# Performance work log

Hardware: AMD Instinct MI355X
Metric: run time of the kernel (lower is better)

Reference implementation:

```python
import jax, jax.numpy as jnp
import numpy as np

DIM = 1024
NUM_HEADS = 16
B, T = 2, 2048


def setup_inputs() -> dict:
    key = jax.random.key(0)
    ks = jax.random.split(key, 7)
    s = 0.02
    return {
        "Q": jax.random.normal(ks[0], (B, T, DIM), dtype=jnp.float32),
        "K": jax.random.normal(ks[1], (B, T, DIM), dtype=jnp.float32),
        "V": jax.random.normal(ks[2], (B, T, DIM), dtype=jnp.float32),
        "Wq": jax.random.normal(ks[3], (DIM, DIM), dtype=jnp.float32) * s,
        "Wk": jax.random.normal(ks[4], (DIM, DIM), dtype=jnp.float32) * s,
        "Wv": jax.random.normal(ks[5], (DIM, DIM), dtype=jnp.float32) * s,
        "Wp": jax.random.normal(ks[6], (DIM, DIM), dtype=jnp.float32) * s,
    }


def _split_heads(x, h):
    b, t, d = x.shape
    return x.reshape(b, t, h, d // h).transpose(0, 2, 1, 3)  # b h t d


def reference(Q, K, V, Wq, Wk, Wv, Wp):
    b, t, d = Q.shape
    h = NUM_HEADS
    # NOTE: module scales by 1/sqrt(dim) (full model dim), not 1/sqrt(head_dim)
    scale = 1.0 / np.sqrt(d).astype(np.float32)
    # torch Linear: x @ W.T (bias=False)
    q = _split_heads(Q @ Wq.T, h)  # b h t hd
    k = _split_heads(K @ Wk.T, h)
    v = _split_heads(V @ Wv.T, h)
    att = jnp.einsum('bhid,bhjd->bhij', q, k) * scale  # b h t t
    causal = jnp.tril(jnp.ones((t, t), dtype=bool))
    att = jnp.where(causal[None, None], att, -jnp.inf)
    att = jax.nn.softmax(att, axis=-1)
    y = jnp.einsum('bhij,bhjd->bhid', att, v)  # b h t hd
    y = y.transpose(0, 2, 1, 3).reshape(b, t, d)
    y = y @ Wp.T
    return (y, att, k, v)
```

## Files before the change

### kernel.cpp

```cpp
#include <hip/hip_runtime.h>

typedef __attribute__((ext_vector_type(8))) short s16x8;
typedef __attribute__((ext_vector_type(4))) float f32x4;

static __device__ __forceinline__ unsigned short f2bf(float f) {
  union { float f; unsigned int u; } v; v.f = f;
  unsigned int u = v.u;
  u += 0x7fffu + ((u >> 16) & 1u);
  return (unsigned short)(u >> 16);
}
static __device__ __forceinline__ void gload16(const void* g, void* l) {
  __builtin_amdgcn_global_load_lds((const __attribute__((address_space(1))) unsigned int*)g,
                                   (__attribute__((address_space(3))) unsigned int*)l, 16, 0, 0);
}

__global__ __launch_bounds__(256) void cast7_bf16(
    const float* __restrict__ i0, const float* __restrict__ i1, const float* __restrict__ i2,
    const float* __restrict__ i3, const float* __restrict__ i4, const float* __restrict__ i5,
    const float* __restrict__ i6,
    unsigned short* __restrict__ o0, unsigned short* __restrict__ o1,
    unsigned short* __restrict__ o2, unsigned short* __restrict__ o3,
    unsigned short* __restrict__ o4, unsigned short* __restrict__ o5,
    unsigned short* __restrict__ o6) {
  const int z = blockIdx.z;
  const float* in = z == 0 ? i0 : z == 1 ? i1 : z == 2 ? i2 : z == 3 ? i3 : z == 4 ? i4
                    : z == 5 ? i5 : i6;
  unsigned short* out = z == 0 ? o0 : z == 1 ? o1 : z == 2 ? o2 : z == 3 ? o3 : z == 4 ? o4
                        : z == 5 ? o5 : o6;
  const int n = (z < 3) ? 4194304 : 1048576;
  int i = (blockIdx.x * 256 + threadIdx.x) * 8;
  if (i >= n) return;
  float4 a = *reinterpret_cast<const float4*>(in + i);
  float4 b = *reinterpret_cast<const float4*>(in + i + 4);
  s16x8 o;
  o[0] = (short)f2bf(a.x); o[1] = (short)f2bf(a.y);
  o[2] = (short)f2bf(a.z); o[3] = (short)f2bf(a.w);
  o[4] = (short)f2bf(b.x); o[5] = (short)f2bf(b.y);
  o[6] = (short)f2bf(b.z); o[7] = (short)f2bf(b.w);
  *reinterpret_cast<s16x8*>(out + i) = o;
}

__global__ __launch_bounds__(256) void gemm_bf16(
    const unsigned short* __restrict__ A0, const unsigned short* __restrict__ A1,
    const unsigned short* __restrict__ A2,
    const unsigned short* __restrict__ W0, const unsigned short* __restrict__ W1,
    const unsigned short* __restrict__ W2,
    unsigned short* __restrict__ Oq, unsigned short* __restrict__ Ok,
    float* __restrict__ Kf, unsigned short* __restrict__ OvT,
    float* __restrict__ Vf, float* __restrict__ Orm) {
  __shared__ __align__(16) char LDS[32768];

  const int z = blockIdx.z;
  const unsigned short* A = z == 0 ? A0 : z == 1 ? A1 : A2;
  const unsigned short* W = z == 0 ? W0 : z == 1 ? W1 : W2;

  const int tid = threadIdx.x, lane = tid & 63, w = tid >> 6;
  const int wm = w >> 1, wn = w & 1;
  const int row0 = blockIdx.y * 128, col0 = blockIdx.x * 128;

  f32x4 acc[4][4];
#pragma unroll
  for (int m = 0; m < 4; ++m)
#pragma unroll
    for (int n = 0; n < 4; ++n) acc[m][n] = f32x4{0.f, 0.f, 0.f, 0.f};

  const int srow = tid >> 3;
  const int swb = ((tid & 7) * 16) ^ ((srow & 7) << 4);
  const unsigned short* aSrc = A + (size_t)(row0 + srow) * 1024 + (swb >> 1);
  const unsigned short* bSrc = W + (size_t)(col0 + srow) * 1024 + (swb >> 1);
  char* ldsA = LDS + w * 1024;
  char* ldsB = LDS + 16384 + w * 1024;

  const int lr = lane & 15, g16 = (lane >> 4) * 16;

  for (int k0 = 0; k0 < 1024; k0 += 64) {
    __syncthreads();
#pragma unroll
    for (int p = 0; p < 4; ++p) gload16(aSrc + (size_t)p * 32 * 1024 + k0, ldsA + p * 4096);
#pragma unroll
    for (int p = 0; p < 4; ++p) gload16(bSrc + (size_t)p * 32 * 1024 + k0, ldsB + p * 4096);
    __syncthreads();

    s16x8 af[2][4], bf[2][4];
#pragma unroll
    for (int ks = 0; ks < 2; ++ks) {
#pragma unroll
      for (int m = 0; m < 4; ++m) {
        int r = wm * 64 + m * 16 + lr;
        int cb = (ks * 64 + g16) ^ ((r & 7) << 4);
        af[ks][m] = *reinterpret_cast<const s16x8*>(LDS + r * 128 + cb);
      }
#pragma unroll
      for (int n = 0; n < 4; ++n) {
        int r = wn * 64 + n * 16 + lr;
        int cb = (ks * 64 + g16) ^ ((r & 7) << 4);
        bf[ks][n] = *reinterpret_cast<const s16x8*>(LDS + 16384 + r * 128 + cb);
      }
    }
#pragma unroll
    for (int ks = 0; ks < 2; ++ks)
#pragma unroll
      for (int m = 0; m < 4; ++m)
#pragma unroll
        for (int n = 0; n < 4; ++n)
          acc[m][n] = __builtin_amdgcn_mfma_f32_16x16x32_bf16(af[ks][m], bf[ks][n], acc[m][n], 0, 0, 0);
  }

  const int er = (lane >> 4) * 4, ec = lane & 15;
  const int b = row0 >> 11, trow = row0 & 2047;

  if (Orm) {
#pragma unroll
    for (int m = 0; m < 4; ++m)
#pragma unroll
      for (int n = 0; n < 4; ++n)
#pragma unroll
        for (int j = 0; j < 4; ++j)
          Orm[(size_t)(row0 + wm * 64 + m * 16 + er + j) * 1024 + col0 + wn * 64 + n * 16 + ec] =
              acc[m][n][j];
    return;
  }

  {
    float* F = (z == 1) ? Kf : (z == 2) ? Vf : nullptr;
    if (F) {
#pragma unroll
      for (int m = 0; m < 4; ++m)
#pragma unroll
        for (int n = 0; n < 4; ++n)
#pragma unroll
          for (int j = 0; j < 4; ++j) {
            int t = trow + wm * 64 + m * 16 + er + j;
            int gd = col0 + wn * 64 + n * 16 + ec;
            F[((size_t)(b * 16 + (gd >> 6)) * 2048 + t) * 64 + (gd & 63)] = acc[m][n][j];
          }
    }
  }

  __syncthreads();
  if (z == 2) {
#pragma unroll
    for (int m = 0; m < 4; ++m)
#pragma unroll
      for (int n = 0; n < 4; ++n)
#pragma unroll
        for (int j = 0; j < 4; ++j) {
          int d = wn * 64 + n * 16 + ec, t = wm * 64 + m * 16 + er + j;
          *reinterpret_cast<short*>(LDS + d * 256 + t * 2) = (short)f2bf(acc[m][n][j]);
        }
    __syncthreads();
    const int dr = tid >> 1, half = tid & 1;
    const int gd = col0 + dr, h = gd >> 6, dd = gd & 63;
    unsigned short* dst = OvT + ((size_t)(b * 16 + h) * 64 + dd) * 2048 + trow + half * 64;
    const char* src = LDS + dr * 256 + half * 128;
#pragma unroll
    for (int i = 0; i < 8; ++i)
      *reinterpret_cast<s16x8*>(dst + i * 8) = *reinterpret_cast<const s16x8*>(src + i * 16);
  } else {
    unsigned short* On = (z == 0) ? Oq : Ok;
#pragma unroll
    for (int m = 0; m < 4; ++m)
#pragma unroll
      for (int n = 0; n < 4; ++n)
#pragma unroll
        for (int j = 0; j < 4; ++j) {
          int r = wm * 64 + m * 16 + er + j, c = wn * 64 + n * 16 + ec;
          *reinterpret_cast<short*>(LDS + r * 256 + c * 2) = (short)f2bf(acc[m][n][j]);
        }
    __syncthreads();
    const int r = tid >> 1, half = tid & 1;
    const int h = (col0 >> 6) + half;
    unsigned short* dst = On + ((size_t)(b * 16 + h) * 2048 + trow + r) * 64;
    const char* src = LDS + r * 256 + half * 128;
#pragma unroll
    for (int i = 0; i < 8; ++i)
      *reinterpret_cast<s16x8*>(dst + i * 8) = *reinterpret_cast<const s16x8*>(src + i * 16);
  }
}

#define ALD 68

__global__ __launch_bounds__(256) void attn_kernel(
    const unsigned short* __restrict__ qw, const unsigned short* __restrict__ kw,
    const unsigned short* __restrict__ vt, float* __restrict__ att_out,
    unsigned short* __restrict__ yb) {
  __shared__ __align__(16) char LDSA[2][16384];
  __shared__ short Pl[4][16 * ALD];

  const int tid = threadIdx.x, lane = tid & 63, w = tid >> 6;
  const int flat = blockIdx.y * 32 + blockIdx.x;
  const int xcd = flat & 7, idx = flat >> 3;
  const int bh = xcd * 4 + (idx >> 5);
  const int iblk = 31 - (idx & 31);
  const float scale2 = 0.03125f * 1.44269504f;

  const int lr = lane & 15, g16 = (lane >> 4) * 16;
  const int lk = (lane >> 4) * 8, er = (lane >> 4) * 4;
  const int rbase = iblk * 64 + w * 16 + er;

  s16x8 aq[2];
  {
    const unsigned short* qb = qw + ((size_t)bh * 2048 + iblk * 64 + w * 16 + lr) * 64;
    aq[0] = *reinterpret_cast<const s16x8*>(qb + lk);
    aq[1] = *reinterpret_cast<const s16x8*>(qb + 32 + lk);
  }

  const int sw = ((lane & 7) * 16) ^ ((lane >> 3) << 4);
  const unsigned short* kLane = kw + (size_t)bh * 131072 + (size_t)(lane >> 3) * 64 + (sw >> 1);
  const unsigned short* vLane = vt + (size_t)bh * 131072 + (size_t)(lane >> 3) * 2048 + (sw >> 1);

  float lrow[4] = {0.f, 0.f, 0.f, 0.f};

  {
    const int npairs = (iblk + 2) >> 1;
#pragma unroll
    for (int i = 0; i < 4; ++i)
      gload16(kLane + (size_t)(w * 32 + i * 8) * 64, LDSA[0] + w * 4096 + i * 1024);
    __syncthreads();
    int buf = 0;
    for (int p = 0; p < npairs; ++p) {
      if (p + 1 < npairs) {
#pragma unroll
        for (int i = 0; i < 4; ++i)
          gload16(kLane + (size_t)((p + 1) * 128 + w * 32 + i * 8) * 64,
                  LDSA[buf ^ 1] + w * 4096 + i * 1024);
      }
#pragma unroll
      for (int sub = 0; sub < 2; ++sub) {
        int jt = 2 * p + sub;
        if (jt > iblk) break;
        const char* Kb = LDSA[buf] + sub * 8192;
        f32x4 s[4];
#pragma unroll
        for (int n = 0; n < 4; ++n) {
          s[n] = f32x4{0.f, 0.f, 0.f, 0.f};
          int r = n * 16 + lr;
#pragma unroll
          for (int ks = 0; ks < 2; ++ks) {
            int cb = (ks * 64 + g16) ^ ((r & 7) << 4);
            s16x8 bK = *reinterpret_cast<const s16x8*>(Kb + r * 128 + cb);
            s[n] = __builtin_amdgcn_mfma_f32_16x16x32_bf16(aq[ks], bK, s[n], 0, 0, 0);
          }
        }
#pragma unroll
        for (int n = 0; n < 4; ++n) {
          int c = jt * 64 + n * 16 + lr;
#pragma unroll
          for (int j = 0; j < 4; ++j) {
            float sv = (c > rbase + j) ? -1e30f : s[n][j] * scale2;
            s[n][j] = __builtin_exp2f(sv);
          }
        }
#pragma unroll
        for (int j = 0; j < 4; ++j)
          lrow[j] += (s[0][j] + s[1][j]) + (s[2][j] + s[3][j]);
      }
      __syncthreads();
      buf ^= 1;
    }
  }

  float rl[4];
#pragma unroll
  for (int j = 0; j < 4; ++j) {
#pragma unroll
    for (int msk = 1; msk < 16; msk <<= 1) lrow[j] += __shfl_xor(lrow[j], msk);
    rl[j] = 1.0f / lrow[j];
  }

  f32x4 yacc[4];
#pragma unroll
  for (int n = 0; n < 4; ++n) yacc[n] = f32x4{0.f, 0.f, 0.f, 0.f};

  {
    gload16(kLane + (size_t)(w * 8) * 64, LDSA[0] + w * 1024);
    gload16(kLane + (size_t)(w * 8 + 32) * 64, LDSA[0] + w * 1024 + 4096);
    gload16(vLane + (size_t)(w * 8) * 2048, LDSA[0] + 8192 + w * 1024);
    gload16(vLane + (size_t)(w * 8 + 32) * 2048, LDSA[0] + 8192 + w * 1024 + 4096);
    __syncthreads();
    int buf = 0;
    for (int jt = 0; jt <= iblk; ++jt) {
      if (jt < iblk) {
        gload16(kLane + (size_t)((jt + 1) * 64 + w * 8) * 64, LDSA[buf ^ 1] + w * 1024);
        gload16(kLane + (size_t)((jt + 1) * 64 + w * 8 + 32) * 64, LDSA[buf ^ 1] + w * 1024 + 4096);
        gload16(vLane + (size_t)(w * 8) * 2048 + (jt + 1) * 64, LDSA[buf ^ 1] + 8192 + w * 1024);
        gload16(vLane + (size_t)(w * 8 + 32) * 2048 + (jt + 1) * 64,
                LDSA[buf ^ 1] + 8192 + w * 1024 + 4096);
      }
      f32x4 s[4];
#pragma unroll
      for (int n = 0; n < 4; ++n) {
        s[n] = f32x4{0.f, 0.f, 0.f, 0.f};
        int r = n * 16 + lr;
#pragma unroll
        for (int ks = 0; ks < 2; ++ks) {
          int cb = (ks * 64 + g16) ^ ((r & 7) << 4);
          s16x8 bK = *reinterpret_cast<const s16x8*>(LDSA[buf] + r * 128 + cb);
          s[n] = __builtin_amdgcn_mfma_f32_16x16x32_bf16(aq[ks], bK, s[n], 0, 0, 0);
        }
      }
#pragma unroll
      for (int n = 0; n < 4; ++n) {
        int c = jt * 64 + n * 16 + lr;
#pragma unroll
        for (int j = 0; j < 4; ++j) {
          float sv = (c > rbase + j) ? -1e30f : s[n][j] * scale2;
          float p = __builtin_exp2f(sv) * rl[j];
          att_out[((size_t)bh * 2048 + rbase + j) * 2048 + c] = p;
          Pl[w][(er + j) * ALD + n * 16 + lr] = (short)f2bf(p);
        }
      }
#pragma unroll
      for (int ks = 0; ks < 2; ++ks) {
        s16x8 ap = *reinterpret_cast<const s16x8*>(&Pl[w][lr * ALD + ks * 32 + lk]);
#pragma unroll
        for (int n = 0; n < 4; ++n) {
          int r = n * 16 + lr;
          int cb = (ks * 64 + g16) ^ ((r & 7) << 4);
          s16x8 bv = *reinterpret_cast<const s16x8*>(LDSA[buf] + 8192 + r * 128 + cb);
          yacc[n] = __builtin_amdgcn_mfma_f32_16x16x32_bf16(ap, bv, yacc[n], 0, 0, 0);
        }
      }
      __syncthreads();
      buf ^= 1;
    }
  }

  const int b = bh >> 4, h = bh & 15;
#pragma unroll
  for (int n = 0; n < 4; ++n)
#pragma unroll
    for (int j = 0; j < 4; ++j)
      Pl[w][(er + j) * ALD + n * 16 + lr] = (short)f2bf(yacc[n][j]);
  {
    const int yr = lane >> 2, ch = lane & 3;
    s16x8 v0 = *reinterpret_cast<const s16x8*>(&Pl[w][yr * ALD + ch * 16]);
    s16x8 v1 = *reinterpret_cast<const s16x8*>(&Pl[w][yr * ALD + ch * 16 + 8]);
    unsigned short* dst = yb + ((size_t)b * 2048 + iblk * 64 + w * 16 + yr) * 1024 + h * 64 + ch * 16;
    *reinterpret_cast<s16x8*>(dst) = v0;
    *reinterpret_cast<s16x8*>(dst + 8) = v1;
  }

  int c0 = (iblk + 1) * 64;
  if (c0 < 2048) {
    int nv = (2048 - c0) >> 2;
    const float4 z4 = make_float4(0.f, 0.f, 0.f, 0.f);
    for (int rr = 0; rr < 64; rr += 4) {
      int r = rr + w;
      float4* dst = reinterpret_cast<float4*>(att_out + ((size_t)bh * 2048 + iblk * 64 + r) * 2048 + c0);
      for (int i = lane; i < nv; i += 64) dst[i] = z4;
    }
  }
}

extern "C" void kernel_launch(void* const* d_in, const int* in_sizes, int n_in,
                              void* d_out, int out_size, void* d_ws, size_t ws_size,
                              hipStream_t stream) {
  (void)in_sizes; (void)n_in; (void)out_size; (void)ws_size;
  const float* Q = (const float*)d_in[0];
  const float* K = (const float*)d_in[1];
  const float* V = (const float*)d_in[2];
  const float* Wq = (const float*)d_in[3];
  const float* Wk = (const float*)d_in[4];
  const float* Wv = (const float*)d_in[5];
  const float* Wp = (const float*)d_in[6];
  float* out = (float*)d_out;

  char* ws = (char*)d_ws;
  const size_t MB = 1024 * 1024;
  unsigned short* qb = (unsigned short*)(ws + 0 * MB);
  unsigned short* kb = (unsigned short*)(ws + 8 * MB);
  unsigned short* vb = (unsigned short*)(ws + 16 * MB);
  unsigned short* wqb = (unsigned short*)(ws + 24 * MB);
  unsigned short* wkb = (unsigned short*)(ws + 26 * MB);
  unsigned short* wvb = (unsigned short*)(ws + 28 * MB);
  unsigned short* wpb = (unsigned short*)(ws + 30 * MB);
  unsigned short* qws = (unsigned short*)(ws + 32 * MB);
  unsigned short* kws = (unsigned short*)(ws + 40 * MB);
  unsigned short* vwt = (unsigned short*)(ws + 48 * MB);
  unsigned short* yb = (unsigned short*)(ws + 0 * MB);

  float* att_out = out + 4194304;
  float* k_out = out + 138412032;
  float* v_out = out + 142606336;

  cast7_bf16<<<dim3(2048, 1, 7), 256, 0, stream>>>(Q, K, V, Wq, Wk, Wv, Wp,
                                                   qb, kb, vb, wqb, wkb, wvb, wpb);

  gemm_bf16<<<dim3(8, 32, 3), 256, 0, stream>>>(qb, kb, vb, wqb, wkb, wvb,
                                                qws, kws, k_out, vwt, v_out, nullptr);

  attn_kernel<<<dim3(32, 32), 256, 0, stream>>>(qws, kws, vwt, att_out, yb);

  gemm_bf16<<<dim3(8, 32, 1), 256, 0, stream>>>(yb, nullptr, nullptr, wpb, nullptr, nullptr,
                                                nullptr, nullptr, nullptr, nullptr, nullptr, out);
}
```

Baseline: 254.4 us.

## Interleave causal zero-fill of mirrored rows into pass one; fold softmax scale into Q

The softmax scale and log2e factor are now applied when the Q projection is written to bf16, so the attention kernel no longer multiplies every score. The causal mask test is limited to the diagonal tile, with a branch-free path for the other tiles. The end-of-kernel zero-fill of the upper triangle of att is replaced by having each block zero the rows of its mirror block (31-iblk), spread across the pass-one loop iterations. Because the mirror's zero region grows with the block's own compute, this aims to balance store traffic across blocks and overlap it with MFMA work. In exchange, Q is rounded to bf16 after scaling, which slightly changes numerics, and the loop carries extra store bookkeeping.

```diff
diff --git a/kernel.cpp b/kernel.cpp
--- a/kernel.cpp
+++ b/kernel.cpp
@@ -158,6 +158,7 @@
       *reinterpret_cast<s16x8*>(dst + i * 8) = *reinterpret_cast<const s16x8*>(src + i * 16);
   } else {
     unsigned short* On = (z == 0) ? Oq : Ok;
+    const float osc = (z == 0) ? 0.04508422f : 1.0f;
 #pragma unroll
     for (int m = 0; m < 4; ++m)
 #pragma unroll
@@ -165,7 +166,7 @@
 #pragma unroll
         for (int j = 0; j < 4; ++j) {
           int r = wm * 64 + m * 16 + er + j, c = wn * 64 + n * 16 + ec;
-          *reinterpret_cast<short*>(LDS + r * 256 + c * 2) = (short)f2bf(acc[m][n][j]);
+          *reinterpret_cast<short*>(LDS + r * 256 + c * 2) = (short)f2bf(acc[m][n][j] * osc);
         }
     __syncthreads();
     const int r = tid >> 1, half = tid & 1;
@@ -192,7 +193,6 @@
   const int xcd = flat & 7, idx = flat >> 3;
   const int bh = xcd * 4 + (idx >> 5);
   const int iblk = 31 - (idx & 31);
-  const float scale2 = 0.03125f * 1.44269504f;
 
   const int lr = lane & 15, g16 = (lane >> 4) * 16;
   const int lk = (lane >> 4) * 8, er = (lane >> 4) * 4;
@@ -209,10 +209,18 @@
   const unsigned short* kLane = kw + (size_t)bh * 131072 + (size_t)(lane >> 3) * 64 + (sw >> 1);
   const unsigned short* vLane = vt + (size_t)bh * 131072 + (size_t)(lane >> 3) * 2048 + (sw >> 1);
 
+  const int zr = 31 - iblk;
+  const int Z = 4 * iblk;
+  const int npairs = (iblk + 2) >> 1;
+  const int zq = (Z + npairs - 1) / npairs;
+  float* zbase = att_out + ((size_t)bh * 2048 + zr * 64 + w * 16 + (lane >> 2)) * 2048;
+  const int zc40 = (((zr + 1) * 64) >> 2) + (lane & 3);
+  int zi = 0;
+  const float4 z4 = make_float4(0.f, 0.f, 0.f, 0.f);
+
   float lrow[4] = {0.f, 0.f, 0.f, 0.f};
 
   {
-    const int npairs = (iblk + 2) >> 1;
 #pragma unroll
     for (int i = 0; i < 4; ++i)
       gload16(kLane + (size_t)(w * 32 + i * 8) * 64, LDSA[0] + w * 4096 + i * 1024);
@@ -242,22 +250,30 @@
             s[n] = __builtin_amdgcn_mfma_f32_16x16x32_bf16(aq[ks], bK, s[n], 0, 0, 0);
           }
         }
-#pragma unroll
-        for (int n = 0; n < 4; ++n) {
-          int c = jt * 64 + n * 16 + lr;
-#pragma unroll
-          for (int j = 0; j < 4; ++j) {
-            float sv = (c > rbase + j) ? -1e30f : s[n][j] * scale2;
-            s[n][j] = __builtin_exp2f(sv);
+        if (jt == iblk) {
+#pragma unroll
+          for (int n = 0; n < 4; ++n) {
+            int c = jt * 64 + n * 16 + lr;
+#pragma unroll
+            for (int j = 0; j < 4; ++j)
+              s[n][j] = __builtin_exp2f((c > rbase + j) ? -1e30f : s[n][j]);
           }
+        } else {
+#pragma unroll
+          for (int n = 0; n < 4; ++n)
+#pragma unroll
+            for (int j = 0; j < 4; ++j) s[n][j] = __builtin_exp2f(s[n][j]);
         }
 #pragma unroll
         for (int j = 0; j < 4; ++j)
           lrow[j] += (s[0][j] + s[1][j]) + (s[2][j] + s[3][j]);
       }
+      for (int e = 0; e < zq && zi < Z; ++e, ++zi)
+        reinterpret_cast<float4*>(zbase)[zc40 + 4 * zi] = z4;
       __syncthreads();
       buf ^= 1;
     }
+    while (zi < Z) { reinterpret_cast<float4*>(zbase)[zc40 + 4 * zi] = z4; ++zi; }
   }
 
   float rl[4];
@@ -299,15 +315,27 @@
           s[n] = __builtin_amdgcn_mfma_f32_16x16x32_bf16(aq[ks], bK, s[n], 0, 0, 0);
         }
       }
-#pragma unroll
-      for (int n = 0; n < 4; ++n) {
-        int c = jt * 64 + n * 16 + lr;
-#pragma unroll
-        for (int j = 0; j < 4; ++j) {
-          float sv = (c > rbase + j) ? -1e30f : s[n][j] * scale2;
-          float p = __builtin_exp2f(sv) * rl[j];
-          att_out[((size_t)bh * 2048 + rbase + j) * 2048 + c] = p;
-          Pl[w][(er + j) * ALD + n * 16 + lr] = (short)f2bf(p);
+      if (jt == iblk) {
+#pragma unroll
+        for (int n = 0; n < 4; ++n) {
+          int c = jt * 64 + n * 16 + lr;
+#pragma unroll
+          for (int j = 0; j < 4; ++j) {
+            float p = __builtin_exp2f((c > rbase + j) ? -1e30f : s[n][j]) * rl[j];
+            att_out[((size_t)bh * 2048 + rbase + j) * 2048 + c] = p;
+            Pl[w][(er + j) * ALD + n * 16 + lr] = (short)f2bf(p);
+          }
+        }
+      } else {
+#pragma unroll
+        for (int n = 0; n < 4; ++n) {
+          int c = jt * 64 + n * 16 + lr;
+#pragma unroll
+          for (int j = 0; j < 4; ++j) {
+            float p = __builtin_exp2f(s[n][j]) * rl[j];
+            att_out[((size_t)bh * 2048 + rbase + j) * 2048 + c] = p;
+            Pl[w][(er + j) * ALD + n * 16 + lr] = (short)f2bf(p);
+          }
         }
       }
 #pragma unroll
@@ -339,17 +367,6 @@
     unsigned short* dst = yb + ((size_t)b * 2048 + iblk * 64 + w * 16 + yr) * 1024 + h * 64 + ch * 16;
     *reinterpret_cast<s16x8*>(dst) = v0;
     *reinterpret_cast<s16x8*>(dst + 8) = v1;
-  }
-
-  int c0 = (iblk + 1) * 64;
-  if (c0 < 2048) {
-    int nv = (2048 - c0) >> 2;
-    const float4 z4 = make_float4(0.f, 0.f, 0.f, 0.f);
-    for (int rr = 0; rr < 64; rr += 4) {
-      int r = rr + w;
-      float4* dst = reinterpret_cast<float4*>(att_out + ((size_t)bh * 2048 + iblk * 64 + r) * 2048 + c0);
-      for (int i = lane; i < nv; i += 64) dst[i] = z4;
-    }
   }
 }
 
```

Measured after the change: 274.8 us. 1.08x slower.
